# Kernel tuning notes

Measured on AMD Instinct MI355X. Metric: run time of the kernel, lower is better.

Reference implementation:

```python
import jax, jax.numpy as jnp
import numpy as np

N_NODES = 100000
N_EDGES = 3200000
IN_DIM, HID_DIM, OUT_DIM = 768, 50, 2


def gcn_conv(x, W, b, row, col, deg_isqrt, n_nodes):
    # PyG GCNConv: h = x @ W, then symmetric-normalized scatter-add (self-loops
    # already included in row/col), then + bias.
    h = x @ W                                    # [N, out]
    norm = deg_isqrt[row] * deg_isqrt[col]       # [E+N]
    msgs = h[row] * norm[:, None]                # gather + scale
    out = jax.ops.segment_sum(msgs, col, num_segments=n_nodes)
    return out + b


def _augment(edge_index, n_nodes):
    # add self-loops and compute D^{-1/2} with self-loops
    loops = jnp.arange(n_nodes, dtype=edge_index.dtype)
    row = jnp.concatenate([edge_index[0], loops])
    col = jnp.concatenate([edge_index[1], loops])
    deg = jax.ops.segment_sum(jnp.ones_like(col, dtype=jnp.float32), col,
                              num_segments=n_nodes)
    deg_isqrt = jnp.where(deg > 0, jax.lax.rsqrt(deg), 0.0)
    return row, col, deg_isqrt


def setup_inputs() -> dict:
    key = jax.random.key(0)
    k1, k2, k3, k4 = jax.random.split(key, 4)
    x = jax.random.normal(k1, (N_NODES, IN_DIM), dtype=jnp.float32)
    edge_index = jax.random.randint(k2, (2, N_EDGES), 0, N_NODES, dtype=jnp.int64)
    W1 = jax.random.normal(k3, (IN_DIM, HID_DIM), dtype=jnp.float32) / np.sqrt(IN_DIM)
    b1 = jnp.zeros((HID_DIM,), dtype=jnp.float32)
    W2 = jax.random.normal(k4, (HID_DIM, OUT_DIM), dtype=jnp.float32) / np.sqrt(HID_DIM)
    b2 = jnp.zeros((OUT_DIM,), dtype=jnp.float32)
    return {"x": x, "edge_index": edge_index, "W1": W1, "b1": b1, "W2": W2, "b2": b2}


def reference(x, edge_index, W1, b1, W2, b2):
    n = x.shape[0]
    row, col, deg_isqrt = _augment(edge_index, n)
    h = gcn_conv(x, W1, b1, row, col, deg_isqrt, n)   # GCNConv(768 -> 50)
    h = jax.nn.relu(h)                                 # ReLU
    h = gcn_conv(h, W2, b2, row, col, deg_isqrt, n)   # GCNConv(50 -> 2)
    return jax.nn.sigmoid(h)                           # Sigmoid output layer
```

## Files before the change

kernel.cpp:

```cpp
#include <hip/hip_runtime.h>


#define N_NODES 100000
#define N_EDGES 3200000
#define IN_DIM  768
#define HID     50
#define HIDP    52
#define SCAN_BLK 1024
#define NSCAN_BLKS 98
#define NPAD (NSCAN_BLKS * SCAN_BLK)
#define NKSTEP (IN_DIM / 32)

using s8v = __attribute__((ext_vector_type(8))) short;
using f4v = __attribute__((ext_vector_type(4))) float;

__device__ __forceinline__ short f2bf(float f) {
  union { float f; unsigned u; } v; v.f = f;
  unsigned r = (v.u + 0x7fffu + ((v.u >> 16) & 1u)) >> 16;
  return (short)r;
}
__device__ __forceinline__ float bf2f(unsigned short u) {
  union { unsigned u; float f; } v; v.u = ((unsigned)u) << 16;
  return v.f;
}


__global__ void k_count(const int* __restrict__ edges, int* __restrict__ cnt) {
  int e = blockIdx.x * 256 + threadIdx.x;
  if (e < N_EDGES) atomicAdd(&cnt[edges[N_EDGES + e]], 1);
}

__global__ void k_scanA(const int* __restrict__ cnt, int* __restrict__ offs,
                        int* __restrict__ bsum) {
  __shared__ int s[SCAN_BLK];
  int t = threadIdx.x;
  int g = blockIdx.x * SCAN_BLK + t;
  int v = (g < N_NODES) ? cnt[g] : 0;
  s[t] = v;
  __syncthreads();
  for (int off = 1; off < SCAN_BLK; off <<= 1) {
    int add = (t >= off) ? s[t - off] : 0;
    __syncthreads();
    s[t] += add;
    __syncthreads();
  }
  offs[g] = s[t] - v;
  if (t == SCAN_BLK - 1) bsum[blockIdx.x] = s[t];
}

__global__ void k_scanB(int* __restrict__ bsum) {
  __shared__ int s[128];
  int t = threadIdx.x;
  int v = (t < NSCAN_BLKS) ? bsum[t] : 0;
  s[t] = v;
  __syncthreads();
  for (int off = 1; off < 128; off <<= 1) {
    int add = (t >= off) ? s[t - off] : 0;
    __syncthreads();
    s[t] += add;
    __syncthreads();
  }
  if (t < NSCAN_BLKS) bsum[t] = s[t] - v;
}

__global__ void k_scanC(int* __restrict__ cnt, int* __restrict__ offs,
                        const int* __restrict__ bsum, float* __restrict__ dis) {
  int g = blockIdx.x * 256 + threadIdx.x;
  if (g < NPAD) {
    offs[g] += bsum[g >> 10];
    if (g < N_NODES) {
      dis[g] = rsqrtf((float)cnt[g] + 1.0f);
      cnt[g] = 0;
    }
  }
}

__global__ void k_fill(const int* __restrict__ edges, int* __restrict__ cnt,
                       const int* __restrict__ offs, int* __restrict__ eidx) {
  int e = blockIdx.x * 256 + threadIdx.x;
  if (e < N_EDGES) {
    int r = edges[e];
    int c = edges[N_EDGES + e];
    int p = atomicAdd(&cnt[c], 1);
    eidx[offs[c] + p] = r;
  }
}


__global__ void k_wprep(const float* __restrict__ W1, short* __restrict__ Bfrag) {
  int g = blockIdx.x * 256 + threadIdx.x;
  int s = g >> 8, r = g & 255;
  int nt = r >> 6, l = r & 63;
  int col = l & 15, quad = l >> 4;
  int n = nt * 16 + col;
  int kb = s * 32 + quad * 8;
  s8v o;
#pragma unroll
  for (int j = 0; j < 8; ++j)
    o[j] = (n < HID) ? f2bf(W1[(size_t)(kb + j) * HID + n]) : (short)0;
  *(s8v*)(Bfrag + (size_t)g * 8) = o;
}


__global__ __launch_bounds__(256) void k_gemm1(const float* __restrict__ x,
                                               const short* __restrict__ Bfrag,
                                               const float* __restrict__ dis,
                                               unsigned short* __restrict__ h1) {
  int t = threadIdx.x;
  int wave = t >> 6, lane = t & 63;
  int col = lane & 15, quad = lane >> 4;
  int rb = blockIdx.x * 64 + wave * 16;
  int arow = rb + col;
  if (arow > N_NODES - 1) arow = N_NODES - 1;
  const float* xrow = x + (size_t)arow * IN_DIM + quad * 8;
  const short* bbase = Bfrag + (size_t)lane * 8;

  f4v acc[4] = {f4v{0.f,0.f,0.f,0.f}, f4v{0.f,0.f,0.f,0.f},
                f4v{0.f,0.f,0.f,0.f}, f4v{0.f,0.f,0.f,0.f}};

#pragma unroll
  for (int s = 0; s < NKSTEP; ++s) {
    float4 va = *(const float4*)(xrow + s * 32);
    float4 vb = *(const float4*)(xrow + s * 32 + 4);
    s8v b0 = *(const s8v*)(bbase + (size_t)(s * 4 + 0) * 512);
    s8v b1 = *(const s8v*)(bbase + (size_t)(s * 4 + 1) * 512);
    s8v b2 = *(const s8v*)(bbase + (size_t)(s * 4 + 2) * 512);
    s8v b3 = *(const s8v*)(bbase + (size_t)(s * 4 + 3) * 512);
    s8v a;
    a[0] = f2bf(va.x); a[1] = f2bf(va.y); a[2] = f2bf(va.z); a[3] = f2bf(va.w);
    a[4] = f2bf(vb.x); a[5] = f2bf(vb.y); a[6] = f2bf(vb.z); a[7] = f2bf(vb.w);
    acc[0] = __builtin_amdgcn_mfma_f32_16x16x32_bf16(a, b0, acc[0], 0, 0, 0);
    acc[1] = __builtin_amdgcn_mfma_f32_16x16x32_bf16(a, b1, acc[1], 0, 0, 0);
    acc[2] = __builtin_amdgcn_mfma_f32_16x16x32_bf16(a, b2, acc[2], 0, 0, 0);
    acc[3] = __builtin_amdgcn_mfma_f32_16x16x32_bf16(a, b3, acc[3], 0, 0, 0);
  }

  int node0 = rb + quad * 4;
  float dd[4];
#pragma unroll
  for (int r = 0; r < 4; ++r)
    dd[r] = (node0 + r < N_NODES) ? dis[node0 + r] : 0.f;
#pragma unroll
  for (int nt = 0; nt < 4; ++nt) {
    int c = nt * 16 + col;
    if (c < HIDP) {
#pragma unroll
      for (int r = 0; r < 4; ++r) {
        int node = node0 + r;
        if (node < N_NODES)
          h1[(size_t)node * HIDP + c] = (unsigned short)f2bf(acc[nt][r] * dd[r]);
      }
    }
  }
}


__global__ __launch_bounds__(256) void k_agg1(
    const unsigned short* __restrict__ h1, const int* __restrict__ eidx,
    const int* __restrict__ offs, const float* __restrict__ dis,
    const float* __restrict__ b1, const float* __restrict__ W2,
    float* __restrict__ h2s) {
  __shared__ float W2s[2][64];
  __shared__ float b1s[64];
  int t = threadIdx.x;
  if (t < 64) {
    b1s[t] = (t < HID) ? b1[t] : 0.f;
    W2s[0][t] = (t < HID) ? W2[t * 2 + 0] : 0.f;
    W2s[1][t] = (t < HID) ? W2[t * 2 + 1] : 0.f;
  }
  __syncthreads();
  int wave = t >> 6, lane = t & 63;
  int n = blockIdx.x * 4 + wave;
  if (n >= N_NODES) return;
  int way = lane >> 4, L = lane & 15;
  int base = L * 4;
  bool actC = base < HIDP;
  int baseS = actC ? base : 0;
  int start = offs[n];
  int end = (n == N_NODES - 1) ? N_EDGES : offs[n + 1];

  float a0 = 0.f, a1 = 0.f, a2 = 0.f, a3 = 0.f;
  int i  = start + way;
  int idx  = (i  < end) ? eidx[i]  : n;
  ushort4 u = *(const ushort4*)(h1 + (size_t)idx * HIDP + baseS);
  int i2 = i + 4;
  int idx2 = (i2 < end) ? eidx[i2] : n;
  while (i < end) {
    ushort4 u2 = *(const ushort4*)(h1 + (size_t)idx2 * HIDP + baseS);
    int i3 = i2 + 4;
    int idx3 = (i3 < end) ? eidx[i3] : n;
    a0 += bf2f(u.x); a1 += bf2f(u.y); a2 += bf2f(u.z); a3 += bf2f(u.w);
    u = u2; idx2 = idx3; i = i2; i2 = i3;
  }

  a0 += __shfl_xor(a0, 16); a0 += __shfl_xor(a0, 32);
  a1 += __shfl_xor(a1, 16); a1 += __shfl_xor(a1, 32);
  a2 += __shfl_xor(a2, 16); a2 += __shfl_xor(a2, 32);
  a3 += __shfl_xor(a3, 16); a3 += __shfl_xor(a3, 32);

  float p0 = 0.f, p1 = 0.f;
  if (actC && way == 0) {
    float dn = dis[n];
    ushort4 us = *(const ushort4*)(h1 + (size_t)n * HIDP + base);
    float s0 = (a0 + bf2f(us.x)) * dn + b1s[base + 0];
    float s1 = (a1 + bf2f(us.y)) * dn + b1s[base + 1];
    float s2 = (a2 + bf2f(us.z)) * dn + b1s[base + 2];
    float s3 = (a3 + bf2f(us.w)) * dn + b1s[base + 3];
    s0 = fmaxf(s0, 0.f); s1 = fmaxf(s1, 0.f);
    s2 = fmaxf(s2, 0.f); s3 = fmaxf(s3, 0.f);
    p0 = s0 * W2s[0][base] + s1 * W2s[0][base + 1] +
         s2 * W2s[0][base + 2] + s3 * W2s[0][base + 3];
    p1 = s0 * W2s[1][base] + s1 * W2s[1][base + 1] +
         s2 * W2s[1][base + 2] + s3 * W2s[1][base + 3];
  }
  for (int m = 8; m; m >>= 1) {
    p0 += __shfl_xor(p0, m, 16);
    p1 += __shfl_xor(p1, m, 16);
  }
  if (lane == 0) {
    float dn = dis[n];
    h2s[(size_t)n * 2 + 0] = p0 * dn;
    h2s[(size_t)n * 2 + 1] = p1 * dn;
  }
}


__global__ __launch_bounds__(256) void k_agg2(
    const float* __restrict__ h2s, const int* __restrict__ eidx,
    const int* __restrict__ offs, const float* __restrict__ dis,
    const float* __restrict__ b2, float* __restrict__ out) {
  int t = threadIdx.x;
  int wave = t >> 6, lane = t & 63;
  int n = blockIdx.x * 4 + wave;
  if (n >= N_NODES) return;
  int start = offs[n];
  int end = (n == N_NODES - 1) ? N_EDGES : offs[n + 1];
  float s0 = 0.f, s1 = 0.f;
  for (int i = start + lane; i < end; i += 64) {
    int idx = eidx[i];
    float2 v = *(const float2*)(h2s + (size_t)idx * 2);
    s0 += v.x; s1 += v.y;
  }
  for (int m = 32; m; m >>= 1) {
    s0 += __shfl_xor(s0, m);
    s1 += __shfl_xor(s1, m);
  }
  if (lane == 0) {
    float dn = dis[n];
    float2 v = *(const float2*)(h2s + (size_t)n * 2);
    float r0 = (s0 + v.x) * dn + b2[0];
    float r1 = (s1 + v.y) * dn + b2[1];
    out[(size_t)n * 2 + 0] = 1.f / (1.f + __expf(-r0));
    out[(size_t)n * 2 + 1] = 1.f / (1.f + __expf(-r1));
  }
}


static inline size_t aln(size_t v) { return (v + 255) & ~(size_t)255; }

extern "C" void kernel_launch(void* const* d_in, const int* in_sizes, int n_in,
                              void* d_out, int out_size, void* d_ws, size_t ws_size,
                              hipStream_t stream) {
  const float* x     = (const float*)d_in[0];
  const int*   edges = (const int*)d_in[1];
  const float* W1    = (const float*)d_in[2];
  const float* b1    = (const float*)d_in[3];
  const float* W2    = (const float*)d_in[4];
  const float* b2    = (const float*)d_in[5];
  float* out = (float*)d_out;

  char* p = (char*)d_ws;
  int* cnt  = (int*)p;            p += aln((size_t)NPAD * 4);
  int* offs = (int*)p;            p += aln((size_t)NPAD * 4);
  int* bsum = (int*)p;            p += aln((size_t)NSCAN_BLKS * 4);
  float* dis = (float*)p;         p += aln((size_t)N_NODES * 4);
  int* eidx = (int*)p;            p += aln((size_t)N_EDGES * 4);
  short* Bfrag = (short*)p;       p += aln((size_t)NKSTEP * 4 * 64 * 8 * 2);
  unsigned short* h1 = (unsigned short*)p; p += aln((size_t)N_NODES * HIDP * 2);
  float* h2s = (float*)p;         p += aln((size_t)N_NODES * 2 * 4);

  int gN   = (NPAD + 255) / 256;
  int gE   = (N_EDGES + 255) / 256;
  int gMM  = (N_NODES + 63) / 64;
  int gW   = (N_NODES + 3) / 4;

  hipMemsetAsync(cnt, 0, (size_t)NPAD * 4, stream);
  k_count<<<gE, 256, 0, stream>>>(edges, cnt);
  k_scanA<<<NSCAN_BLKS, SCAN_BLK, 0, stream>>>(cnt, offs, bsum);
  k_scanB<<<1, 128, 0, stream>>>(bsum);
  k_scanC<<<gN, 256, 0, stream>>>(cnt, offs, bsum, dis);
  k_fill <<<gE, 256, 0, stream>>>(edges, cnt, offs, eidx);
  k_wprep<<<NKSTEP, 256, 0, stream>>>(W1, Bfrag);
  k_gemm1<<<gMM, 256, 0, stream>>>(x, Bfrag, dis, h1);
  k_agg1 <<<gW, 256, 0, stream>>>(h1, eidx, offs, dis, b1, W2, h2s);
  k_agg2 <<<gW, 256, 0, stream>>>(h2s, eidx, offs, dis, b2, out);
}
```

Baseline: 839.2 us.

## Record atomic slot in count pass and double rows per wave in GEMM

After: 780.7 us. -7.0%, faster.

```diff
diff --git a/kernel.cpp b/kernel.cpp
--- a/kernel.cpp
+++ b/kernel.cpp
@@ -25,9 +25,10 @@
 }
 
 
-__global__ void k_count(const int* __restrict__ edges, int* __restrict__ cnt) {
+__global__ void k_count(const int* __restrict__ edges, int* __restrict__ cnt,
+                        int* __restrict__ pos) {
   int e = blockIdx.x * 256 + threadIdx.x;
-  if (e < N_EDGES) atomicAdd(&cnt[edges[N_EDGES + e]], 1);
+  if (e < N_EDGES) pos[e] = atomicAdd(&cnt[edges[N_EDGES + e]], 1);
 }
 
 __global__ void k_scanA(const int* __restrict__ cnt, int* __restrict__ offs,
@@ -63,26 +64,22 @@
   if (t < NSCAN_BLKS) bsum[t] = s[t] - v;
 }
 
-__global__ void k_scanC(int* __restrict__ cnt, int* __restrict__ offs,
+__global__ void k_scanC(const int* __restrict__ cnt, int* __restrict__ offs,
                         const int* __restrict__ bsum, float* __restrict__ dis) {
   int g = blockIdx.x * 256 + threadIdx.x;
   if (g < NPAD) {
     offs[g] += bsum[g >> 10];
-    if (g < N_NODES) {
+    if (g < N_NODES)
       dis[g] = rsqrtf((float)cnt[g] + 1.0f);
-      cnt[g] = 0;
-    }
-  }
-}
-
-__global__ void k_fill(const int* __restrict__ edges, int* __restrict__ cnt,
+  }
+}
+
+__global__ void k_fill(const int* __restrict__ edges, const int* __restrict__ pos,
                        const int* __restrict__ offs, int* __restrict__ eidx) {
   int e = blockIdx.x * 256 + threadIdx.x;
   if (e < N_EDGES) {
-    int r = edges[e];
     int c = edges[N_EDGES + e];
-    int p = atomicAdd(&cnt[c], 1);
-    eidx[offs[c] + p] = r;
+    eidx[offs[c] + pos[e]] = edges[e];
   }
 }
 
@@ -109,46 +106,63 @@
   int t = threadIdx.x;
   int wave = t >> 6, lane = t & 63;
   int col = lane & 15, quad = lane >> 4;
-  int rb = blockIdx.x * 64 + wave * 16;
-  int arow = rb + col;
-  if (arow > N_NODES - 1) arow = N_NODES - 1;
-  const float* xrow = x + (size_t)arow * IN_DIM + quad * 8;
+  int rb = blockIdx.x * 128 + wave * 32;
+  int arow0 = rb + col;
+  int arow1 = rb + 16 + col;
+  if (arow0 > N_NODES - 1) arow0 = N_NODES - 1;
+  if (arow1 > N_NODES - 1) arow1 = N_NODES - 1;
+  const float* xrow0 = x + (size_t)arow0 * IN_DIM + quad * 8;
+  const float* xrow1 = x + (size_t)arow1 * IN_DIM + quad * 8;
   const short* bbase = Bfrag + (size_t)lane * 8;
 
-  f4v acc[4] = {f4v{0.f,0.f,0.f,0.f}, f4v{0.f,0.f,0.f,0.f},
+  f4v acc[8] = {f4v{0.f,0.f,0.f,0.f}, f4v{0.f,0.f,0.f,0.f},
+                f4v{0.f,0.f,0.f,0.f}, f4v{0.f,0.f,0.f,0.f},
+                f4v{0.f,0.f,0.f,0.f}, f4v{0.f,0.f,0.f,0.f},
                 f4v{0.f,0.f,0.f,0.f}, f4v{0.f,0.f,0.f,0.f}};
 
 #pragma unroll
   for (int s = 0; s < NKSTEP; ++s) {
-    float4 va = *(const float4*)(xrow + s * 32);
-    float4 vb = *(const float4*)(xrow + s * 32 + 4);
+    float4 va0 = *(const float4*)(xrow0 + s * 32);
+    float4 vb0 = *(const float4*)(xrow0 + s * 32 + 4);
+    float4 va1 = *(const float4*)(xrow1 + s * 32);
+    float4 vb1 = *(const float4*)(xrow1 + s * 32 + 4);
     s8v b0 = *(const s8v*)(bbase + (size_t)(s * 4 + 0) * 512);
     s8v b1 = *(const s8v*)(bbase + (size_t)(s * 4 + 1) * 512);
     s8v b2 = *(const s8v*)(bbase + (size_t)(s * 4 + 2) * 512);
     s8v b3 = *(const s8v*)(bbase + (size_t)(s * 4 + 3) * 512);
-    s8v a;
-    a[0] = f2bf(va.x); a[1] = f2bf(va.y); a[2] = f2bf(va.z); a[3] = f2bf(va.w);
-    a[4] = f2bf(vb.x); a[5] = f2bf(vb.y); a[6] = f2bf(vb.z); a[7] = f2bf(vb.w);
-    acc[0] = __builtin_amdgcn_mfma_f32_16x16x32_bf16(a, b0, acc[0], 0, 0, 0);
-    acc[1] = __builtin_amdgcn_mfma_f32_16x16x32_bf16(a, b1, acc[1], 0, 0, 0);
-    acc[2] = __builtin_amdgcn_mfma_f32_16x16x32_bf16(a, b2, acc[2], 0, 0, 0);
-    acc[3] = __builtin_amdgcn_mfma_f32_16x16x32_bf16(a, b3, acc[3], 0, 0, 0);
-  }
-
-  int node0 = rb + quad * 4;
-  float dd[4];
-#pragma unroll
-  for (int r = 0; r < 4; ++r)
-    dd[r] = (node0 + r < N_NODES) ? dis[node0 + r] : 0.f;
-#pragma unroll
-  for (int nt = 0; nt < 4; ++nt) {
-    int c = nt * 16 + col;
-    if (c < HIDP) {
-#pragma unroll
-      for (int r = 0; r < 4; ++r) {
-        int node = node0 + r;
-        if (node < N_NODES)
-          h1[(size_t)node * HIDP + c] = (unsigned short)f2bf(acc[nt][r] * dd[r]);
+    s8v a0, a1;
+    a0[0] = f2bf(va0.x); a0[1] = f2bf(va0.y); a0[2] = f2bf(va0.z); a0[3] = f2bf(va0.w);
+    a0[4] = f2bf(vb0.x); a0[5] = f2bf(vb0.y); a0[6] = f2bf(vb0.z); a0[7] = f2bf(vb0.w);
+    a1[0] = f2bf(va1.x); a1[1] = f2bf(va1.y); a1[2] = f2bf(va1.z); a1[3] = f2bf(va1.w);
+    a1[4] = f2bf(vb1.x); a1[5] = f2bf(vb1.y); a1[6] = f2bf(vb1.z); a1[7] = f2bf(vb1.w);
+    acc[0] = __builtin_amdgcn_mfma_f32_16x16x32_bf16(a0, b0, acc[0], 0, 0, 0);
+    acc[1] = __builtin_amdgcn_mfma_f32_16x16x32_bf16(a0, b1, acc[1], 0, 0, 0);
+    acc[2] = __builtin_amdgcn_mfma_f32_16x16x32_bf16(a0, b2, acc[2], 0, 0, 0);
+    acc[3] = __builtin_amdgcn_mfma_f32_16x16x32_bf16(a0, b3, acc[3], 0, 0, 0);
+    acc[4] = __builtin_amdgcn_mfma_f32_16x16x32_bf16(a1, b0, acc[4], 0, 0, 0);
+    acc[5] = __builtin_amdgcn_mfma_f32_16x16x32_bf16(a1, b1, acc[5], 0, 0, 0);
+    acc[6] = __builtin_amdgcn_mfma_f32_16x16x32_bf16(a1, b2, acc[6], 0, 0, 0);
+    acc[7] = __builtin_amdgcn_mfma_f32_16x16x32_bf16(a1, b3, acc[7], 0, 0, 0);
+  }
+
+#pragma unroll
+  for (int half = 0; half < 2; ++half) {
+    int node0 = rb + half * 16 + quad * 4;
+    float dd[4];
+#pragma unroll
+    for (int r = 0; r < 4; ++r)
+      dd[r] = (node0 + r < N_NODES) ? dis[node0 + r] : 0.f;
+#pragma unroll
+    for (int nt = 0; nt < 4; ++nt) {
+      int c = nt * 16 + col;
+      if (c < HIDP) {
+#pragma unroll
+        for (int r = 0; r < 4; ++r) {
+          int node = node0 + r;
+          if (node < N_NODES)
+            h1[(size_t)node * HIDP + c] =
+                (unsigned short)f2bf(acc[half * 4 + nt][r] * dd[r]);
+        }
       }
     }
   }
@@ -275,21 +289,22 @@
   int* bsum = (int*)p;            p += aln((size_t)NSCAN_BLKS * 4);
   float* dis = (float*)p;         p += aln((size_t)N_NODES * 4);
   int* eidx = (int*)p;            p += aln((size_t)N_EDGES * 4);
+  int* pos  = (int*)p;            p += aln((size_t)N_EDGES * 4);
   short* Bfrag = (short*)p;       p += aln((size_t)NKSTEP * 4 * 64 * 8 * 2);
   unsigned short* h1 = (unsigned short*)p; p += aln((size_t)N_NODES * HIDP * 2);
   float* h2s = (float*)p;         p += aln((size_t)N_NODES * 2 * 4);
 
   int gN   = (NPAD + 255) / 256;
   int gE   = (N_EDGES + 255) / 256;
-  int gMM  = (N_NODES + 63) / 64;
+  int gMM  = (N_NODES + 127) / 128;
   int gW   = (N_NODES + 3) / 4;
 
-  hipMemsetAsync(cnt, 0, (size_t)NPAD * 4, stream);
-  k_count<<<gE, 256, 0, stream>>>(edges, cnt);
+  hipMemsetAsync(cnt, 0, (size_t)N_NODES * 4, stream);
+  k_count<<<gE, 256, 0, stream>>>(edges, cnt, pos);
   k_scanA<<<NSCAN_BLKS, SCAN_BLK, 0, stream>>>(cnt, offs, bsum);
   k_scanB<<<1, 128, 0, stream>>>(bsum);
   k_scanC<<<gN, 256, 0, stream>>>(cnt, offs, bsum, dis);
-  k_fill <<<gE, 256, 0, stream>>>(edges, cnt, offs, eidx);
+  k_fill <<<gE, 256, 0, stream>>>(edges, pos, offs, eidx);
   k_wprep<<<NKSTEP, 256, 0, stream>>>(W1, Bfrag);
   k_gemm1<<<gMM, 256, 0, stream>>>(x, Bfrag, dis, h1);
   k_agg1 <<<gW, 256, 0, stream>>>(h1, eidx, offs, dis, b1, W2, h2s);
```
